# Kernel optimization log

Measured on AMD Instinct MI355X. Metric: run time of the kernel, lower is better.

The kernel has to match this reference:

```python
import jax, jax.numpy as jnp
import numpy as np

D = 196; NCH = 64; H = 8; DH = 64; INNER = H * DH; MLP = 784; SEQ = 65


def _ln(x, g, b, eps=1e-5):
    m = x.mean(-1, keepdims=True)
    v = x.var(-1, keepdims=True)
    return (x - m) / jnp.sqrt(v + eps) * g + b


def setup_inputs() -> dict:
    key = jax.random.key(0)
    ks = jax.random.split(key, 12)
    f = jax.random.normal
    return dict(
        x=f(ks[0], (1, SEQ, D), dtype=jnp.float32),
        tokens=f(ks[1], (1, D), dtype=jnp.float32),
        x_pe=f(ks[2], (1, NCH, D), dtype=jnp.float32),
        conv_k=f(ks[3], (3, 3), dtype=jnp.float32) * 0.3,   # Conv2d(1,1,3) kernel
        bn_g=jnp.ones(()), bn_b=jnp.zeros(()), bn_rm=jnp.zeros(()), bn_rv=jnp.ones(()),
        fc_w1=f(ks[4], (NCH, 12)) * 0.1,
        fc_w2=f(ks[5], (12, NCH)) * 0.1,
        ln1_g=jnp.ones((D,)), ln1_b=jnp.zeros((D,)),
        ln2_g=jnp.ones((D,)), ln2_b=jnp.zeros((D,)),
        w_qkv=f(ks[6], (D, 3 * INNER)) * 0.05,
        w_out=f(ks[7], (INNER, D)) * 0.05, b_out=jnp.zeros((D,)),
        ff_w1=f(ks[8], (D, MLP)) * 0.05, ff_b1=jnp.zeros((MLP,)),
        ff_w2=f(ks[9], (MLP, D)) * 0.05, ff_b2=jnp.zeros((D,)),
    )


def reference(x, tokens, x_pe, conv_k, bn_g, bn_b, bn_rm, bn_rv,
              fc_w1, fc_w2, ln1_g, ln1_b, ln2_g, ln2_b,
              w_qkv, w_out, b_out, ff_w1, ff_b1, ff_w2, ff_b2):
    # --- per-channel Conv2d(1,1,3,p=1)+BN+ReLU, batched over all 64 rows ---
    # Each row is (1,1,1,196): height 1 with pad 1 means the top/bottom kernel
    # rows only touch zero padding, so only the middle kernel row contributes
    # -> equivalent to a 1D conv with kernel conv_k[1].
    rows = x_pe[0]                      # [64,196]
    km = conv_k[1]                      # [3]
    xp = jnp.pad(rows, ((0, 0), (1, 1)))
    conv = km[0] * xp[:, :D] + km[1] * xp[:, 1:D + 1] + km[2] * xp[:, 2:D + 2]
    bn = (conv - bn_rm) / jnp.sqrt(bn_rv + 1e-5) * bn_g + bn_b
    a = jax.nn.relu(bn)                 # [64,196]  (== x_AfterConv / a)

    # --- sort-based suppress/excitation channel gating ---
    b1 = a.mean(-1)                     # [64] adaptive avg pool
    val = jnp.sort(b1)
    idx = jnp.argsort(b1)
    middle = jnp.where((val.max() < 0) | (val.min() > 0),
                       jnp.int32(32), jnp.argmax(val > 0).astype(jnp.int32))
    rank = jnp.argsort(idx)             # rank of each channel in ascending order
    sup = rank < middle                 # channels in idx[:middle]
    l_s = middle.astype(b1.dtype)
    l_e = (NCH - middle).astype(b1.dtype)
    b2 = jnp.where(sup,
                   b1 - 1.0 / (1.0 + jnp.power(l_s, b1)),
                   b1 + 1.0 / (1.0 + jnp.power(l_e, -b1)))

    c = jax.nn.sigmoid(jax.nn.relu(b2 @ fc_w1) @ fc_w2)   # [64]
    x_att = a * c[:, None]                                  # [64,196]
    x_att = jnp.concatenate([x_att, tokens.reshape(1, D)], axis=0)[None]  # [1,65,196]

    # --- PreNorm attention ---
    h = _ln(x, ln1_g, ln1_b)
    qkv = h @ w_qkv
    q, k, v = jnp.split(qkv, 3, axis=-1)
    def heads(t):
        return t.reshape(1, SEQ, H, DH).transpose(0, 2, 1, 3)  # b h n d
    q, k, v = heads(q), heads(k), heads(v)
    attn = jax.nn.softmax(jnp.einsum('bhnd,bhmd->bhnm', q, k) * (DH ** -0.5), axis=-1)
    o = jnp.einsum('bhnm,bhmd->bhnd', attn, v).transpose(0, 2, 1, 3).reshape(1, SEQ, INNER)
    x = o @ w_out + b_out + x + x_att

    # --- PreNorm feed-forward ---
    h2 = _ln(x, ln2_g, ln2_b)
    x = (jax.nn.gelu(h2 @ ff_w1 + ff_b1, approximate=False) @ ff_w2 + ff_b2) + x
    return x
```

## Files before the change

### kernel.cpp

```cpp
#include <hip/hip_runtime.h>
#include <math.h>

#define D 196
#define NCH 64
#define NH 8
#define DHD 64
#define INNER 512
#define MLP 784
#define SEQ 65

__device__ __forceinline__ float bsum(float v, float* red) {
    for (int off = 32; off > 0; off >>= 1) v += __shfl_down(v, off, 64);
    int lane = threadIdx.x & 63, wid = threadIdx.x >> 6;
    if (lane == 0) red[wid] = v;
    __syncthreads();
    float s = red[0] + red[1] + red[2] + red[3];
    __syncthreads();
    return s;
}

__global__ void __launch_bounds__(256) k1(const float* __restrict__ x_pe,
        const float* __restrict__ conv_k, const float* __restrict__ bn_g,
        const float* __restrict__ bn_b, const float* __restrict__ bn_rm,
        const float* __restrict__ bn_rv, const float* __restrict__ x,
        const float* __restrict__ ln1_g, const float* __restrict__ ln1_b,
        const float* __restrict__ w_qkv,
        float* __restrict__ a, float* __restrict__ b1, float* __restrict__ qkv,
        float* __restrict__ out) {
    __shared__ float red[4];
    __shared__ float h[D];
    __shared__ float ps[512];
    int b = blockIdx.x, t = threadIdx.x;
    if (b < NCH) {
        int zi = b * 200 + t;
        if (t < 200 && zi < SEQ * D) out[zi] = 0.f;
        const float* row = x_pe + b * D;
        float val = 0.f;
        if (t < D) {
            float km0 = conv_k[3], km1 = conv_k[4], km2 = conv_k[5];
            float inv = rsqrtf(bn_rv[0] + 1e-5f);
            float l = (t > 0) ? row[t - 1] : 0.f;
            float m = row[t];
            float r = (t < D - 1) ? row[t + 1] : 0.f;
            float conv = km0 * l + km1 * m + km2 * r;
            float bn = (conv - bn_rm[0]) * inv * bn_g[0] + bn_b[0];
            val = fmaxf(bn, 0.f);
            a[b * D + t] = val;
        }
        float tot = bsum(val, red);
        if (t == 0) b1[b] = tot * (1.f / (float)D);
    } else {
        int qb = b - NCH;
        int n = qb / 12, cg = qb % 12;
        const float* row = x + n * D;
        float v = (t < D) ? row[t] : 0.f;
        float mean = bsum(v, red) * (1.f / (float)D);
        float d = (t < D) ? (v - mean) : 0.f;
        float var = bsum(d * d, red) * (1.f / (float)D);
        float rinv = rsqrtf(var + 1e-5f);
        if (t < D) h[t] = d * rinv * ln1_g[t] + ln1_b[t];
        __syncthreads();
        int qq = t >> 6, lt = t & 63;
        int c0 = cg * 128 + lt * 2;
        const float* wp = w_qkv + (qq * 49) * 1536 + c0;
        const float* hp = h + qq * 49;
        float a0 = 0.f, a1 = 0.f;
#pragma unroll
        for (int i = 0; i < 49; i++) {
            float2 w2 = *(const float2*)(wp + i * 1536);
            float hv = hp[i];
            a0 += hv * w2.x;
            a1 += hv * w2.y;
        }
        ps[qq * 128 + lt * 2] = a0;
        ps[qq * 128 + lt * 2 + 1] = a1;
        __syncthreads();
        if (t < 64) {
            float s0 = ps[t * 2] + ps[128 + t * 2] + ps[256 + t * 2] + ps[384 + t * 2];
            float s1 = ps[t * 2 + 1] + ps[129 + t * 2] + ps[257 + t * 2] + ps[385 + t * 2];
            float2 o2 = make_float2(s0, s1);
            *(float2*)(qkv + n * 1536 + cg * 128 + t * 2) = o2;
        }
    }
}

__global__ void __launch_bounds__(512) k2(const float* __restrict__ b1,
        const float* __restrict__ fc_w1, const float* __restrict__ fc_w2,
        const float* __restrict__ qkv, const float* __restrict__ w_out,
        const float* __restrict__ b_out, const float* __restrict__ x,
        float* __restrict__ c, float* __restrict__ x2) {
    int b = blockIdx.x, t = threadIdx.x;
    if (b == SEQ) {
        __shared__ float sb1[NCH];
        __shared__ float sb2[NCH];
        __shared__ float hid[12];
        if (t < NCH) sb1[t] = b1[t];
        __syncthreads();
        if (t < NCH) {
            float v = sb1[t];
            float mx = -1e30f, mn = 1e30f;
            int cle = 0, rank = 0;
            for (int j = 0; j < NCH; j++) {
                float w = sb1[j];
                mx = fmaxf(mx, w);
                mn = fminf(mn, w);
                if (w <= 0.f) cle++;
                if (w < v || (w == v && j < t)) rank++;
            }
            int middle;
            if (mx < 0.f || mn > 0.f) middle = 32;
            else if (mx <= 0.f) middle = 0;
            else middle = cle;
            float b2;
            if (rank < middle) {
                float ls = (float)middle;
                b2 = v - 1.f / (1.f + powf(ls, v));
            } else {
                float le = (float)(NCH - middle);
                b2 = v + 1.f / (1.f + powf(le, -v));
            }
            sb2[t] = b2;
        }
        __syncthreads();
        if (t < 12) {
            float s = 0.f;
            for (int j = 0; j < NCH; j++) s += sb2[j] * fc_w1[j * 12 + t];
            hid[t] = fmaxf(s, 0.f);
        }
        __syncthreads();
        if (t < NCH) {
            float s = 0.f;
            for (int k = 0; k < 12; k++) s += hid[k] * fc_w2[k * NCH + t];
            c[t] = 1.f / (1.f + expf(-s));
        }
        return;
    }
    __shared__ float sq[512];
    __shared__ float pp[8 * 80];
    __shared__ float so[512];
    __shared__ float ps[784];
    int n = b;
    int w = t >> 6, L = t & 63;
    sq[t] = qkv[n * 1536 + t];
    __syncthreads();
    const float scale = 0.125f;
    const float4* kr = (const float4*)(qkv + L * 1536 + INNER + w * DHD);
    const float4* q4 = (const float4*)(sq + w * DHD);
    float s = 0.f;
#pragma unroll
    for (int i = 0; i < 16; i++) {
        float4 kv = kr[i];
        float4 qv = q4[i];
        s += qv.x * kv.x + qv.y * kv.y + qv.z * kv.z + qv.w * kv.w;
    }
    float sL = s * scale;
    float t64 = sq[w * DHD + L] * qkv[64 * 1536 + INNER + w * DHD + L];
#pragma unroll
    for (int off = 1; off < 64; off <<= 1) t64 += __shfl_xor(t64, off, 64);
    float s64 = t64 * scale;
    float mx = sL;
#pragma unroll
    for (int off = 1; off < 64; off <<= 1) mx = fmaxf(mx, __shfl_xor(mx, off, 64));
    mx = fmaxf(mx, s64);
    float e = expf(sL - mx);
    float e64 = expf(s64 - mx);
    float esum = e;
#pragma unroll
    for (int off = 1; off < 64; off <<= 1) esum += __shfl_xor(esum, off, 64);
    esum += e64;
    float rs = 1.f / esum;
    pp[w * 80 + L] = e;
    if (L == 0) pp[w * 80 + 64] = e64;
    __syncthreads();
    float acc = 0.f;
#pragma unroll 13
    for (int m = 0; m < SEQ; m++)
        acc += pp[w * 80 + m] * qkv[m * 1536 + 2 * INNER + w * DHD + L];
    so[w * DHD + L] = acc * rs;
    __syncthreads();
    if (t < 392) {
        int qq = t / 98, p = t - qq * 98;
        const float* wp = w_out + (qq * 128) * D + 2 * p;
        const float* op = so + qq * 128;
        float a0 = 0.f, a1 = 0.f;
#pragma unroll 16
        for (int i = 0; i < 128; i++) {
            float2 w2 = *(const float2*)(wp + i * D);
            float ov = op[i];
            a0 += ov * w2.x;
            a1 += ov * w2.y;
        }
        ps[qq * 196 + 2 * p] = a0;
        ps[qq * 196 + 2 * p + 1] = a1;
    }
    __syncthreads();
    if (t < 98) {
        float s0 = ps[2 * t] + ps[196 + 2 * t] + ps[392 + 2 * t] + ps[588 + 2 * t];
        float s1 = ps[2 * t + 1] + ps[197 + 2 * t] + ps[393 + 2 * t] + ps[589 + 2 * t];
        float2 xr = *(const float2*)(x + n * D + 2 * t);
        float2 br = *(const float2*)(b_out + 2 * t);
        float2 o2 = make_float2(s0 + xr.x + br.x, s1 + xr.y + br.y);
        *(float2*)(x2 + n * D + 2 * t) = o2;
    }
}

__global__ void __launch_bounds__(256) k3(const float* __restrict__ x2,
        const float* __restrict__ a, const float* __restrict__ c,
        const float* __restrict__ tokens,
        const float* __restrict__ ln2_g, const float* __restrict__ ln2_b,
        const float* __restrict__ ff_w1, const float* __restrict__ ff_b1,
        float* __restrict__ tb) {
    __shared__ float red[4];
    __shared__ float h[D];
    __shared__ float ps[392];
    int n = blockIdx.x, cg = blockIdx.y, t = threadIdx.x;
    float v = 0.f;
    if (t < D) {
        float att = (n < NCH) ? a[n * D + t] * c[n] : tokens[t];
        v = x2[n * D + t] + att;
    }
    float mean = bsum(v, red) * (1.f / (float)D);
    float d = (t < D) ? (v - mean) : 0.f;
    float var = bsum(d * d, red) * (1.f / (float)D);
    float rinv = rsqrtf(var + 1e-5f);
    if (t < D) h[t] = d * rinv * ln2_g[t] + ln2_b[t];
    __syncthreads();
    if (t < D) {
        int qq = t / 49, p = t - qq * 49;
        int c0 = cg * 98 + 2 * p;
        const float* wp = ff_w1 + (qq * 49) * MLP + c0;
        const float* hp = h + qq * 49;
        float a0 = 0.f, a1 = 0.f;
#pragma unroll
        for (int i = 0; i < 49; i++) {
            float2 w2 = *(const float2*)(wp + i * MLP);
            float hv = hp[i];
            a0 += hv * w2.x;
            a1 += hv * w2.y;
        }
        if (qq == 0) { a0 += ff_b1[c0]; a1 += ff_b1[c0 + 1]; }
        ps[qq * 98 + 2 * p] = a0;
        ps[qq * 98 + 2 * p + 1] = a1;
    }
    __syncthreads();
    if (t < 49) {
        float s0 = ps[2 * t] + ps[98 + 2 * t] + ps[196 + 2 * t] + ps[294 + 2 * t];
        float s1 = ps[2 * t + 1] + ps[99 + 2 * t] + ps[197 + 2 * t] + ps[295 + 2 * t];
        float g0 = 0.5f * s0 * (1.f + erff(s0 * 0.70710678118f));
        float g1 = 0.5f * s1 * (1.f + erff(s1 * 0.70710678118f));
        *(float2*)(tb + n * MLP + cg * 98 + 2 * t) = make_float2(g0, g1);
    }
}

__global__ void __launch_bounds__(256) k4(const float* __restrict__ tb,
        const float* __restrict__ ff_w2, const float* __restrict__ ff_b2,
        const float* __restrict__ x2, const float* __restrict__ a,
        const float* __restrict__ c, const float* __restrict__ tokens,
        float* __restrict__ out) {
    __shared__ float st[98];
    __shared__ float ps[392];
    int n = blockIdx.x, kc = blockIdx.y, t = threadIdx.x;
    if (t < 98) st[t] = tb[n * MLP + kc * 98 + t];
    __syncthreads();
    if (t < D) {
        int hh = t / 98, p = t - hh * 98;
        const float* wp = ff_w2 + (kc * 98 + hh * 49) * D + 2 * p;
        const float* sp = st + hh * 49;
        float a0 = 0.f, a1 = 0.f;
#pragma unroll
        for (int i = 0; i < 49; i++) {
            float2 w2 = *(const float2*)(wp + i * D);
            float sv = sp[i];
            a0 += sv * w2.x;
            a1 += sv * w2.y;
        }
        ps[hh * 196 + 2 * p] = a0;
        ps[hh * 196 + 2 * p + 1] = a1;
    }
    __syncthreads();
    if (t < 98) {
        float s0 = ps[2 * t] + ps[196 + 2 * t];
        float s1 = ps[2 * t + 1] + ps[197 + 2 * t];
        if (kc == 0) {
            int c0 = 2 * t;
            float att0 = (n < NCH) ? a[n * D + c0] * c[n] : tokens[c0];
            float att1 = (n < NCH) ? a[n * D + c0 + 1] * c[n] : tokens[c0 + 1];
            s0 += ff_b2[c0] + x2[n * D + c0] + att0;
            s1 += ff_b2[c0 + 1] + x2[n * D + c0 + 1] + att1;
        }
        atomicAdd(&out[n * D + 2 * t], s0);
        atomicAdd(&out[n * D + 2 * t + 1], s1);
    }
}

extern "C" void kernel_launch(void* const* d_in, const int* in_sizes, int n_in,
                              void* d_out, int out_size, void* d_ws, size_t ws_size,
                              hipStream_t stream) {
    const float* x      = (const float*)d_in[0];
    const float* tokens = (const float*)d_in[1];
    const float* x_pe   = (const float*)d_in[2];
    const float* conv_k = (const float*)d_in[3];
    const float* bn_g   = (const float*)d_in[4];
    const float* bn_b   = (const float*)d_in[5];
    const float* bn_rm  = (const float*)d_in[6];
    const float* bn_rv  = (const float*)d_in[7];
    const float* fc_w1  = (const float*)d_in[8];
    const float* fc_w2  = (const float*)d_in[9];
    const float* ln1_g  = (const float*)d_in[10];
    const float* ln1_b  = (const float*)d_in[11];
    const float* ln2_g  = (const float*)d_in[12];
    const float* ln2_b  = (const float*)d_in[13];
    const float* w_qkv  = (const float*)d_in[14];
    const float* w_out  = (const float*)d_in[15];
    const float* b_out  = (const float*)d_in[16];
    const float* ff_w1  = (const float*)d_in[17];
    const float* ff_b1  = (const float*)d_in[18];
    const float* ff_w2  = (const float*)d_in[19];
    const float* ff_b2  = (const float*)d_in[20];
    float* out = (float*)d_out;

    float* ws = (float*)d_ws;
    float* a    = ws;
    float* b1   = ws + 12544;
    float* cc   = ws + 12608;
    float* qkv  = ws + 12672;
    float* x2   = ws + 112512;
    float* tb   = ws + 125252;

    k1<<<844, 256, 0, stream>>>(x_pe, conv_k, bn_g, bn_b, bn_rm, bn_rv,
                                x, ln1_g, ln1_b, w_qkv, a, b1, qkv, out);
    k2<<<SEQ + 1, 512, 0, stream>>>(b1, fc_w1, fc_w2, qkv, w_out, b_out, x, cc, x2);
    k3<<<dim3(SEQ, 8), 256, 0, stream>>>(x2, a, cc, tokens, ln2_g, ln2_b,
                                         ff_w1, ff_b1, tb);
    k4<<<dim3(SEQ, 8), 256, 0, stream>>>(tb, ff_w2, ff_b2, x2, a, cc, tokens, out);
}
```

Measured before the change: 130.1 us.

## Fuse gating, attention, out-proj and full MLP into one per-row kernel

```diff
diff --git a/kernel.cpp b/kernel.cpp
--- a/kernel.cpp
+++ b/kernel.cpp
@@ -9,12 +9,24 @@
 #define MLP 784
 #define SEQ 65
 
-__device__ __forceinline__ float bsum(float v, float* red) {
+__device__ __forceinline__ float bsum256(float v, float* red) {
     for (int off = 32; off > 0; off >>= 1) v += __shfl_down(v, off, 64);
     int lane = threadIdx.x & 63, wid = threadIdx.x >> 6;
     if (lane == 0) red[wid] = v;
     __syncthreads();
     float s = red[0] + red[1] + red[2] + red[3];
+    __syncthreads();
+    return s;
+}
+
+__device__ __forceinline__ float bsum512(float v, float* red) {
+    for (int off = 32; off > 0; off >>= 1) v += __shfl_down(v, off, 64);
+    int lane = threadIdx.x & 63, wid = threadIdx.x >> 6;
+    if (lane == 0) red[wid] = v;
+    __syncthreads();
+    float s = 0.f;
+#pragma unroll
+    for (int i = 0; i < 8; i++) s += red[i];
     __syncthreads();
     return s;
 }
@@ -25,15 +37,12 @@
         const float* __restrict__ bn_rv, const float* __restrict__ x,
         const float* __restrict__ ln1_g, const float* __restrict__ ln1_b,
         const float* __restrict__ w_qkv,
-        float* __restrict__ a, float* __restrict__ b1, float* __restrict__ qkv,
-        float* __restrict__ out) {
+        float* __restrict__ a, float* __restrict__ b1, float* __restrict__ qkv) {
     __shared__ float red[4];
     __shared__ float h[D];
     __shared__ float ps[512];
     int b = blockIdx.x, t = threadIdx.x;
     if (b < NCH) {
-        int zi = b * 200 + t;
-        if (t < 200 && zi < SEQ * D) out[zi] = 0.f;
         const float* row = x_pe + b * D;
         float val = 0.f;
         if (t < D) {
@@ -47,16 +56,16 @@
             val = fmaxf(bn, 0.f);
             a[b * D + t] = val;
         }
-        float tot = bsum(val, red);
+        float tot = bsum256(val, red);
         if (t == 0) b1[b] = tot * (1.f / (float)D);
     } else {
         int qb = b - NCH;
         int n = qb / 12, cg = qb % 12;
         const float* row = x + n * D;
         float v = (t < D) ? row[t] : 0.f;
-        float mean = bsum(v, red) * (1.f / (float)D);
+        float mean = bsum256(v, red) * (1.f / (float)D);
         float d = (t < D) ? (v - mean) : 0.f;
-        float var = bsum(d * d, red) * (1.f / (float)D);
+        float var = bsum256(d * d, red) * (1.f / (float)D);
         float rinv = rsqrtf(var + 1e-5f);
         if (t < D) h[t] = d * rinv * ln1_g[t] + ln1_b[t];
         __syncthreads();
@@ -78,8 +87,7 @@
         if (t < 64) {
             float s0 = ps[t * 2] + ps[128 + t * 2] + ps[256 + t * 2] + ps[384 + t * 2];
             float s1 = ps[t * 2 + 1] + ps[129 + t * 2] + ps[257 + t * 2] + ps[385 + t * 2];
-            float2 o2 = make_float2(s0, s1);
-            *(float2*)(qkv + n * 1536 + cg * 128 + t * 2) = o2;
+            *(float2*)(qkv + n * 1536 + cg * 128 + t * 2) = make_float2(s0, s1);
         }
     }
 }
@@ -88,61 +96,30 @@
         const float* __restrict__ fc_w1, const float* __restrict__ fc_w2,
         const float* __restrict__ qkv, const float* __restrict__ w_out,
         const float* __restrict__ b_out, const float* __restrict__ x,
-        float* __restrict__ c, float* __restrict__ x2) {
-    int b = blockIdx.x, t = threadIdx.x;
-    if (b == SEQ) {
-        __shared__ float sb1[NCH];
-        __shared__ float sb2[NCH];
-        __shared__ float hid[12];
-        if (t < NCH) sb1[t] = b1[t];
-        __syncthreads();
-        if (t < NCH) {
-            float v = sb1[t];
-            float mx = -1e30f, mn = 1e30f;
-            int cle = 0, rank = 0;
-            for (int j = 0; j < NCH; j++) {
-                float w = sb1[j];
-                mx = fmaxf(mx, w);
-                mn = fminf(mn, w);
-                if (w <= 0.f) cle++;
-                if (w < v || (w == v && j < t)) rank++;
-            }
-            int middle;
-            if (mx < 0.f || mn > 0.f) middle = 32;
-            else if (mx <= 0.f) middle = 0;
-            else middle = cle;
-            float b2;
-            if (rank < middle) {
-                float ls = (float)middle;
-                b2 = v - 1.f / (1.f + powf(ls, v));
-            } else {
-                float le = (float)(NCH - middle);
-                b2 = v + 1.f / (1.f + powf(le, -v));
-            }
-            sb2[t] = b2;
-        }
-        __syncthreads();
-        if (t < 12) {
-            float s = 0.f;
-            for (int j = 0; j < NCH; j++) s += sb2[j] * fc_w1[j * 12 + t];
-            hid[t] = fmaxf(s, 0.f);
-        }
-        __syncthreads();
-        if (t < NCH) {
-            float s = 0.f;
-            for (int k = 0; k < 12; k++) s += hid[k] * fc_w2[k * NCH + t];
-            c[t] = 1.f / (1.f + expf(-s));
-        }
-        return;
-    }
+        const float* __restrict__ a, const float* __restrict__ tokens,
+        const float* __restrict__ ln2_g, const float* __restrict__ ln2_b,
+        const float* __restrict__ ff_w1, const float* __restrict__ ff_b1,
+        const float* __restrict__ ff_w2, const float* __restrict__ ff_b2,
+        float* __restrict__ out) {
     __shared__ float sq[512];
+    __shared__ float so[512];
     __shared__ float pp[8 * 80];
-    __shared__ float so[512];
     __shared__ float ps[784];
-    int n = b;
+    __shared__ float sb1[NCH];
+    __shared__ float sb2[NCH];
+    __shared__ float hid[12];
+    __shared__ float cn_s;
+    __shared__ float x2r[200];
+    __shared__ float h[200];
+    __shared__ float tbr[MLP];
+    __shared__ float red[8];
+    int n = blockIdx.x, t = threadIdx.x;
     int w = t >> 6, L = t & 63;
+
     sq[t] = qkv[n * 1536 + t];
-    __syncthreads();
+    if (t < NCH) sb1[t] = b1[t];
+    __syncthreads();
+
     const float scale = 0.125f;
     const float4* kr = (const float4*)(qkv + L * 1536 + INNER + w * DHD);
     const float4* q4 = (const float4*)(sq + w * DHD);
@@ -178,6 +155,7 @@
         acc += pp[w * 80 + m] * qkv[m * 1536 + 2 * INNER + w * DHD + L];
     so[w * DHD + L] = acc * rs;
     __syncthreads();
+
     if (t < 392) {
         int qq = t / 98, p = t - qq * 98;
         const float* wp = w_out + (qq * 128) * D + 2 * p;
@@ -192,104 +170,109 @@
         }
         ps[qq * 196 + 2 * p] = a0;
         ps[qq * 196 + 2 * p + 1] = a1;
-    }
-    __syncthreads();
-    if (t < 98) {
-        float s0 = ps[2 * t] + ps[196 + 2 * t] + ps[392 + 2 * t] + ps[588 + 2 * t];
-        float s1 = ps[2 * t + 1] + ps[197 + 2 * t] + ps[393 + 2 * t] + ps[589 + 2 * t];
-        float2 xr = *(const float2*)(x + n * D + 2 * t);
-        float2 br = *(const float2*)(b_out + 2 * t);
-        float2 o2 = make_float2(s0 + xr.x + br.x, s1 + xr.y + br.y);
-        *(float2*)(x2 + n * D + 2 * t) = o2;
-    }
-}
-
-__global__ void __launch_bounds__(256) k3(const float* __restrict__ x2,
-        const float* __restrict__ a, const float* __restrict__ c,
-        const float* __restrict__ tokens,
-        const float* __restrict__ ln2_g, const float* __restrict__ ln2_b,
-        const float* __restrict__ ff_w1, const float* __restrict__ ff_b1,
-        float* __restrict__ tb) {
-    __shared__ float red[4];
-    __shared__ float h[D];
-    __shared__ float ps[392];
-    int n = blockIdx.x, cg = blockIdx.y, t = threadIdx.x;
+    } else if (t < 456) {
+        int i = t - 392;
+        float v = sb1[i];
+        float gmx = -1e30f, gmn = 1e30f;
+        int cle = 0, rank = 0;
+        for (int j = 0; j < NCH; j++) {
+            float wv = sb1[j];
+            gmx = fmaxf(gmx, wv);
+            gmn = fminf(gmn, wv);
+            if (wv <= 0.f) cle++;
+            if (wv < v || (wv == v && j < i)) rank++;
+        }
+        int middle;
+        if (gmx < 0.f || gmn > 0.f) middle = 32;
+        else if (gmx <= 0.f) middle = 0;
+        else middle = cle;
+        float b2v;
+        if (rank < middle) {
+            float ls = (float)middle;
+            b2v = v - 1.f / (1.f + powf(ls, v));
+        } else {
+            float le = (float)(NCH - middle);
+            b2v = v + 1.f / (1.f + powf(le, -v));
+        }
+        sb2[i] = b2v;
+    }
+    __syncthreads();
+
+    if (t < 12) {
+        float sh = 0.f;
+        for (int j = 0; j < NCH; j++) sh += sb2[j] * fc_w1[j * 12 + t];
+        hid[t] = fmaxf(sh, 0.f);
+    } else if (t >= 128 && t < 226) {
+        int p = t - 128;
+        float s0 = ps[2 * p] + ps[196 + 2 * p] + ps[392 + 2 * p] + ps[588 + 2 * p];
+        float s1 = ps[2 * p + 1] + ps[197 + 2 * p] + ps[393 + 2 * p] + ps[589 + 2 * p];
+        float2 xr = *(const float2*)(x + n * D + 2 * p);
+        float2 br = *(const float2*)(b_out + 2 * p);
+        x2r[2 * p] = s0 + xr.x + br.x;
+        x2r[2 * p + 1] = s1 + xr.y + br.y;
+    }
+    __syncthreads();
+
+    if (t == 0) {
+        float sc = 0.f;
+        for (int k = 0; k < 12; k++) sc += hid[k] * fc_w2[k * NCH + n];
+        cn_s = 1.f / (1.f + expf(-sc));
+    }
+    __syncthreads();
+
     float v = 0.f;
     if (t < D) {
-        float att = (n < NCH) ? a[n * D + t] * c[n] : tokens[t];
-        v = x2[n * D + t] + att;
-    }
-    float mean = bsum(v, red) * (1.f / (float)D);
+        float att = (n < NCH) ? a[n * D + t] * cn_s : tokens[t];
+        v = x2r[t] + att;
+        x2r[t] = v;
+    }
+    float mean = bsum512(v, red) * (1.f / (float)D);
     float d = (t < D) ? (v - mean) : 0.f;
-    float var = bsum(d * d, red) * (1.f / (float)D);
+    float var = bsum512(d * d, red) * (1.f / (float)D);
     float rinv = rsqrtf(var + 1e-5f);
     if (t < D) h[t] = d * rinv * ln2_g[t] + ln2_b[t];
     __syncthreads();
-    if (t < D) {
-        int qq = t / 49, p = t - qq * 49;
-        int c0 = cg * 98 + 2 * p;
-        const float* wp = ff_w1 + (qq * 49) * MLP + c0;
-        const float* hp = h + qq * 49;
-        float a0 = 0.f, a1 = 0.f;
-#pragma unroll
-        for (int i = 0; i < 49; i++) {
+
+    if (t < 392) {
+        const float* wp = ff_w1 + 2 * t;
+        float2 bb = *(const float2*)(ff_b1 + 2 * t);
+        float a0 = bb.x, a1 = bb.y;
+#pragma unroll 28
+        for (int i = 0; i < D; i++) {
             float2 w2 = *(const float2*)(wp + i * MLP);
-            float hv = hp[i];
+            float hv = h[i];
             a0 += hv * w2.x;
             a1 += hv * w2.y;
         }
-        if (qq == 0) { a0 += ff_b1[c0]; a1 += ff_b1[c0 + 1]; }
-        ps[qq * 98 + 2 * p] = a0;
-        ps[qq * 98 + 2 * p + 1] = a1;
-    }
-    __syncthreads();
-    if (t < 49) {
-        float s0 = ps[2 * t] + ps[98 + 2 * t] + ps[196 + 2 * t] + ps[294 + 2 * t];
-        float s1 = ps[2 * t + 1] + ps[99 + 2 * t] + ps[197 + 2 * t] + ps[295 + 2 * t];
-        float g0 = 0.5f * s0 * (1.f + erff(s0 * 0.70710678118f));
-        float g1 = 0.5f * s1 * (1.f + erff(s1 * 0.70710678118f));
-        *(float2*)(tb + n * MLP + cg * 98 + 2 * t) = make_float2(g0, g1);
-    }
-}
-
-__global__ void __launch_bounds__(256) k4(const float* __restrict__ tb,
-        const float* __restrict__ ff_w2, const float* __restrict__ ff_b2,
-        const float* __restrict__ x2, const float* __restrict__ a,
-        const float* __restrict__ c, const float* __restrict__ tokens,
-        float* __restrict__ out) {
-    __shared__ float st[98];
-    __shared__ float ps[392];
-    int n = blockIdx.x, kc = blockIdx.y, t = threadIdx.x;
-    if (t < 98) st[t] = tb[n * MLP + kc * 98 + t];
-    __syncthreads();
-    if (t < D) {
-        int hh = t / 98, p = t - hh * 98;
-        const float* wp = ff_w2 + (kc * 98 + hh * 49) * D + 2 * p;
-        const float* sp = st + hh * 49;
+        tbr[2 * t] = 0.5f * a0 * (1.f + erff(a0 * 0.70710678118f));
+        tbr[2 * t + 1] = 0.5f * a1 * (1.f + erff(a1 * 0.70710678118f));
+    }
+    __syncthreads();
+
+    if (t < 392) {
+        int qq = t / 98, p = t - qq * 98;
+        const float* wp = ff_w2 + (qq * 196) * D + 2 * p;
+        const float* sp = tbr + qq * 196;
         float a0 = 0.f, a1 = 0.f;
-#pragma unroll
-        for (int i = 0; i < 49; i++) {
+#pragma unroll 28
+        for (int i = 0; i < 196; i++) {
             float2 w2 = *(const float2*)(wp + i * D);
             float sv = sp[i];
             a0 += sv * w2.x;
             a1 += sv * w2.y;
         }
-        ps[hh * 196 + 2 * p] = a0;
-        ps[hh * 196 + 2 * p + 1] = a1;
-    }
-    __syncthreads();
+        ps[qq * 196 + 2 * p] = a0;
+        ps[qq * 196 + 2 * p + 1] = a1;
+    }
+    __syncthreads();
+
     if (t < 98) {
-        float s0 = ps[2 * t] + ps[196 + 2 * t];
-        float s1 = ps[2 * t + 1] + ps[197 + 2 * t];
-        if (kc == 0) {
-            int c0 = 2 * t;
-            float att0 = (n < NCH) ? a[n * D + c0] * c[n] : tokens[c0];
-            float att1 = (n < NCH) ? a[n * D + c0 + 1] * c[n] : tokens[c0 + 1];
-            s0 += ff_b2[c0] + x2[n * D + c0] + att0;
-            s1 += ff_b2[c0 + 1] + x2[n * D + c0 + 1] + att1;
-        }
-        atomicAdd(&out[n * D + 2 * t], s0);
-        atomicAdd(&out[n * D + 2 * t + 1], s1);
+        float s0 = ps[2 * t] + ps[196 + 2 * t] + ps[392 + 2 * t] + ps[588 + 2 * t];
+        float s1 = ps[2 * t + 1] + ps[197 + 2 * t] + ps[393 + 2 * t] + ps[589 + 2 * t];
+        float2 bb = *(const float2*)(ff_b2 + 2 * t);
+        float o0 = s0 + bb.x + x2r[2 * t];
+        float o1 = s1 + bb.y + x2r[2 * t + 1];
+        *(float2*)(out + n * D + 2 * t) = make_float2(o0, o1);
     }
 }
 
@@ -322,15 +305,10 @@
     float* ws = (float*)d_ws;
     float* a    = ws;
     float* b1   = ws + 12544;
-    float* cc   = ws + 12608;
-    float* qkv  = ws + 12672;
-    float* x2   = ws + 112512;
-    float* tb   = ws + 125252;
+    float* qkv  = ws + 12608;
 
     k1<<<844, 256, 0, stream>>>(x_pe, conv_k, bn_g, bn_b, bn_rm, bn_rv,
-                                x, ln1_g, ln1_b, w_qkv, a, b1, qkv, out);
-    k2<<<SEQ + 1, 512, 0, stream>>>(b1, fc_w1, fc_w2, qkv, w_out, b_out, x, cc, x2);
-    k3<<<dim3(SEQ, 8), 256, 0, stream>>>(x2, a, cc, tokens, ln2_g, ln2_b,
-                                         ff_w1, ff_b1, tb);
-    k4<<<dim3(SEQ, 8), 256, 0, stream>>>(tb, ff_w2, ff_b2, x2, a, cc, tokens, out);
-}
+                                x, ln1_g, ln1_b, w_qkv, a, b1, qkv);
+    k2<<<SEQ, 512, 0, stream>>>(b1, fc_w1, fc_w2, qkv, w_out, b_out, x, a, tokens,
+                                ln2_g, ln2_b, ff_w1, ff_b1, ff_w2, ff_b2, out);
+}
```

New measurement: 141.2 us. +8.5%, slower.
